# Kernel optimization log

Hardware: AMD Instinct MI355X
Metric: run time of the kernel (lower is better)

The kernel has to match this reference:

```python
import jax, jax.numpy as jnp
import numpy as np

B, S, D = 2, 2048, 1024
H, HD = 16, 64  # num_heads, head_dim; D == H*HD


def setup_inputs() -> dict:
    key = jax.random.key(0)
    k_x, k_wa, k_wp = jax.random.split(key, 3)
    x = jax.random.normal(k_x, (B, S, D), dtype=jnp.float32)
    w_attn = jax.random.normal(k_wa, (D, 3 * D), dtype=jnp.float32) * (1.0 / np.sqrt(D))
    b_attn = jnp.zeros((3 * D,), dtype=jnp.float32)
    w_proj = jax.random.normal(k_wp, (D, D), dtype=jnp.float32) * (1.0 / np.sqrt(D))
    b_proj = jnp.zeros((D,), dtype=jnp.float32)
    return {"x": x, "w_attn": w_attn, "b_attn": b_attn, "w_proj": w_proj, "b_proj": b_proj}


def reference(x, w_attn, b_attn, w_proj, b_proj):
    # c_attn: [B,S,D] -> [B,S,3D], split into q,k,v
    qkv = jnp.einsum('bsd,df->bsf', x, w_attn) + b_attn
    q, k, v = jnp.split(qkv, 3, axis=-1)
    # split heads: [B,S,D] -> [B,S,H,HD]
    q = q.reshape(B, S, H, HD)
    k = k.reshape(B, S, H, HD)
    v = v.reshape(B, S, H, HD)
    scale = 1.0 / jnp.sqrt(jnp.float32(HD))
    # scores: [B,H,S,S]
    scores = jnp.einsum('bnhd,bmhd->bhnm', q, k) * scale
    causal_mask = jnp.tril(jnp.ones((S, S), dtype=jnp.bool_))
    scores = jnp.where(causal_mask, scores, jnp.float32(-1e9))
    attn = jax.nn.softmax(scores, axis=-1)
    # dropout is identity (inference=True / p=0)
    out = jnp.einsum('bhnm,bmhd->bnhd', attn, v)
    out = out.reshape(B, S, D)
    out = jnp.einsum('bsd,de->bse', out, w_proj) + b_proj
    return out
```

## Files before the change

kernel.cpp:

```cpp
#include <hip/hip_runtime.h>

#define Bn 2
#define Sn 2048
#define Dn 1024
#define Hn 16
#define HDn 64

typedef unsigned short u16;
typedef u16 u16x4 __attribute__((ext_vector_type(4)));
typedef u16 u16x8 __attribute__((ext_vector_type(8)));
typedef __bf16 bf16x8 __attribute__((ext_vector_type(8)));
typedef float f32x4 __attribute__((ext_vector_type(4)));

__device__ __forceinline__ u16 f2bf(float f) {
  union { float f; unsigned u; } v; v.f = f;
  unsigned r = v.u + 0x7fffu + ((v.u >> 16) & 1u);
  return (u16)(r >> 16);
}

__device__ __forceinline__ f32x4 mfma16(u16x8 a, u16x8 b, f32x4 c) {
  return __builtin_amdgcn_mfma_f32_16x16x32_bf16(
      __builtin_bit_cast(bf16x8, a), __builtin_bit_cast(bf16x8, b), c, 0, 0, 0);
}

__device__ __forceinline__ int swzb(int row, int bytecol) {
  return row * 128 + (bytecol ^ ((((row & 7) ^ ((row >> 3) & 7))) << 4));
}

__global__ __launch_bounds__(256) void k_cvt(const float* __restrict__ in,
                                             u16* __restrict__ out, int n4) {
  int i = blockIdx.x * 256 + threadIdx.x;
  if (i < n4) {
    const float4 v = reinterpret_cast<const float4*>(in)[i];
    u16x4 o = {f2bf(v.x), f2bf(v.y), f2bf(v.z), f2bf(v.w)};
    reinterpret_cast<u16x4*>(out)[i] = o;
  }
}

__global__ __launch_bounds__(256) void k_transpose(const float* __restrict__ in,
                                                   u16* __restrict__ out,
                                                   int K, int N) {
  __shared__ u16 tile[32][33];
  const int n0 = blockIdx.x * 32, k0 = blockIdx.y * 32;
  const int tx = threadIdx.x, ty = threadIdx.y;
#pragma unroll
  for (int r = 0; r < 4; ++r) {
    const int k = ty * 4 + r;
    tile[k][tx] = f2bf(in[(size_t)(k0 + k) * N + n0 + tx]);
  }
  __syncthreads();
#pragma unroll
  for (int r = 0; r < 4; ++r) {
    const int n = ty * 4 + r;
    out[(size_t)(n0 + n) * K + k0 + tx] = tile[tx][n];
  }
}

__global__ __launch_bounds__(256) void k_gemm_bt(
    const u16* __restrict__ A, const u16* __restrict__ Bt, int K,
    const float* __restrict__ bias, u16* __restrict__ oq, u16* __restrict__ ok,
    u16* __restrict__ ov, float* __restrict__ of, int mode) {
  __shared__ __align__(16) u16 a_lds[128 * 32];
  __shared__ __align__(16) u16 b_lds[128 * 32];
  const int tid = threadIdx.x;
  const int lane = tid & 63, w = tid >> 6;
  const int wr = w >> 1, wc = w & 1;
  const int lm = lane & 15, lk = lane >> 4;
  const int m0 = blockIdx.y * 128, n0 = blockIdx.x * 128;

  f32x4 acc[4][4] = {};

  for (int k0 = 0; k0 < K; k0 += 32) {
#pragma unroll
    for (int p = 0; p < 2; ++p) {
      const int e = p * 2048 + w * 512 + lane * 8;
      const int row = e >> 5, col = e & 31;
      __builtin_amdgcn_global_load_lds(
          (const __attribute__((address_space(1))) void*)(A + (size_t)(m0 + row) * K + k0 + col),
          (__attribute__((address_space(3))) void*)(a_lds + p * 2048 + w * 512),
          16, 0, 0);
      __builtin_amdgcn_global_load_lds(
          (const __attribute__((address_space(1))) void*)(Bt + (size_t)(n0 + row) * K + k0 + col),
          (__attribute__((address_space(3))) void*)(b_lds + p * 2048 + w * 512),
          16, 0, 0);
    }
    __syncthreads();
    u16x8 av[4], bv[4];
#pragma unroll
    for (int m = 0; m < 4; ++m)
      av[m] = *reinterpret_cast<const u16x8*>(a_lds + (wr * 64 + m * 16 + lm) * 32 + lk * 8);
#pragma unroll
    for (int n = 0; n < 4; ++n)
      bv[n] = *reinterpret_cast<const u16x8*>(b_lds + (wc * 64 + n * 16 + lm) * 32 + lk * 8);
#pragma unroll
    for (int m = 0; m < 4; ++m)
#pragma unroll
      for (int n = 0; n < 4; ++n)
        acc[m][n] = mfma16(av[m], bv[n], acc[m][n]);
    __syncthreads();
  }

#pragma unroll
  for (int m = 0; m < 4; ++m) {
#pragma unroll
    for (int n = 0; n < 4; ++n) {
      const int col = n0 + wc * 64 + n * 16 + lm;
      const float bb = bias[col];
#pragma unroll
      for (int j = 0; j < 4; ++j) {
        const int row = m0 + wr * 64 + m * 16 + lk * 4 + j;
        float val = acc[m][n][j] + bb;
        if (mode == 0) {
          const int which = col >> 10;
          const int h = (col >> 6) & 15, hd = col & 63;
          if (which == 0) val *= 0.125f;
          const int b = row >> 11, s = row & 2047;
          const size_t idx = (((size_t)(b * Hn + h)) * Sn + s) * HDn + hd;
          u16* dst = which == 0 ? oq : (which == 1 ? ok : ov);
          dst[idx] = f2bf(val);
        } else {
          of[(size_t)row * Dn + col] = val;
        }
      }
    }
  }
}

__global__ __launch_bounds__(256) void k_attn(const u16* __restrict__ qb,
                                              const u16* __restrict__ kb,
                                              const u16* __restrict__ vb,
                                              u16* __restrict__ ob) {
  const int bx = blockIdx.x;
  const int qt = 31 - (bx >> 5);
  const int bh = bx & 31;
  const int h = bh & 15, b = bh >> 4;
  const int tid = threadIdx.x, lane = tid & 63, w = tid >> 6;
  const int lm = lane & 15, lk = lane >> 4;
  const int Q0 = qt * 64;
  const int q0 = Q0 + w * 16;
  const size_t head = (size_t)(b * Hn + h) * Sn * HDn;
  const u16* Q = qb + head;
  const u16* Kp = kb + head;
  const u16* Vp = vb + head;

  __shared__ __align__(16) u16 k_lds[64 * 64];
  __shared__ __align__(16) u16 vt_lds[64 * 64];
  __shared__ __align__(16) u16 p_lds[4][16 * 64];
  char* myp = (char*)p_lds[w];

  const int sr = tid >> 2, scb = (tid & 3) * 16;
  const u16* Ksrc = Kp + (size_t)sr * HDn + scb;
  const u16* Vsrc = Vp + (size_t)sr * HDn + scb;

  u16x8 aq[2];
#pragma unroll
  for (int c = 0; c < 2; ++c)
    aq[c] = *reinterpret_cast<const u16x8*>(Q + (size_t)(q0 + lm) * HDn + c * 32 + lk * 8);

  f32x4 o_acc[4] = {};
  float mrow = -1e30f, lrow = 0.f;
  const float C = 1.44269504f;

  const int nk = Q0 + 64;
  u16x8 kreg[2], vreg[2];
  kreg[0] = *reinterpret_cast<const u16x8*>(Ksrc);
  kreg[1] = *reinterpret_cast<const u16x8*>(Ksrc + 8);
  vreg[0] = *reinterpret_cast<const u16x8*>(Vsrc);
  vreg[1] = *reinterpret_cast<const u16x8*>(Vsrc + 8);

  for (int j0 = 0; j0 < nk; j0 += 64) {
    *reinterpret_cast<u16x8*>((char*)k_lds + swzb(sr, scb * 2)) = kreg[0];
    *reinterpret_cast<u16x8*>((char*)k_lds + swzb(sr, scb * 2 + 16)) = kreg[1];
#pragma unroll
    for (int i = 0; i < 8; ++i) {
      *reinterpret_cast<u16*>((char*)vt_lds + swzb(scb + i, sr * 2)) = vreg[0][i];
      *reinterpret_cast<u16*>((char*)vt_lds + swzb(scb + 8 + i, sr * 2)) = vreg[1][i];
    }
    __syncthreads();
    if (j0 + 64 < nk) {
      const u16* kn = Ksrc + (size_t)(j0 + 64) * HDn;
      const u16* vn = Vsrc + (size_t)(j0 + 64) * HDn;
      kreg[0] = *reinterpret_cast<const u16x8*>(kn);
      kreg[1] = *reinterpret_cast<const u16x8*>(kn + 8);
      vreg[0] = *reinterpret_cast<const u16x8*>(vn);
      vreg[1] = *reinterpret_cast<const u16x8*>(vn + 8);
    }

    f32x4 s[4];
#pragma unroll
    for (int kc = 0; kc < 4; ++kc) {
      const u16x8 kf0 = *reinterpret_cast<const u16x8*>((char*)k_lds + swzb(kc * 16 + lm, lk * 16));
      const u16x8 kf1 = *reinterpret_cast<const u16x8*>((char*)k_lds + swzb(kc * 16 + lm, 64 + lk * 16));
      f32x4 z = {};
      z = mfma16(kf0, aq[0], z);
      s[kc] = mfma16(kf1, aq[1], z);
    }
    if (j0 + 63 > q0) {
#pragma unroll
      for (int kc = 0; kc < 4; ++kc)
#pragma unroll
        for (int jj = 0; jj < 4; ++jj)
          if (j0 + kc * 16 + lk * 4 + jj > q0 + lm) s[kc][jj] = -1e30f;
    }

    float vmax = -1e30f;
#pragma unroll
    for (int kc = 0; kc < 4; ++kc)
#pragma unroll
      for (int jj = 0; jj < 4; ++jj) vmax = fmaxf(vmax, s[kc][jj]);
    vmax = fmaxf(vmax, __shfl_xor(vmax, 16, 64));
    vmax = fmaxf(vmax, __shfl_xor(vmax, 32, 64));
    const float mnew = fmaxf(mrow, vmax);
    const float alpha = exp2f((mrow - mnew) * C);
    mrow = mnew;
    const float mc = mnew * C;
    float psum = 0.f;
#pragma unroll
    for (int kc = 0; kc < 4; ++kc) {
      u16x4 pk;
#pragma unroll
      for (int jj = 0; jj < 4; ++jj) {
        const float p = exp2f(s[kc][jj] * C - mc);
        psum += p;
        pk[jj] = f2bf(p);
      }
      *reinterpret_cast<u16x4*>(myp + swzb(lm, kc * 32 + lk * 8)) = pk;
    }
    psum += __shfl_xor(psum, 16, 64);
    psum += __shfl_xor(psum, 32, 64);
    lrow = lrow * alpha + psum;

    float a4[4];
#pragma unroll
    for (int jj = 0; jj < 4; ++jj) a4[jj] = __shfl(alpha, lk * 4 + jj, 64);
#pragma unroll
    for (int t = 0; t < 4; ++t)
#pragma unroll
      for (int jj = 0; jj < 4; ++jj) o_acc[t][jj] *= a4[jj];

#pragma unroll
    for (int kt = 0; kt < 2; ++kt) {
      const u16x8 pa = *reinterpret_cast<const u16x8*>(myp + swzb(lm, kt * 64 + lk * 16));
#pragma unroll
      for (int t = 0; t < 4; ++t) {
        const u16x8 vf = *reinterpret_cast<const u16x8*>((char*)vt_lds + swzb(t * 16 + lm, kt * 64 + lk * 16));
        o_acc[t] = mfma16(pa, vf, o_acc[t]);
      }
    }
    __syncthreads();
  }

  float l4[4];
#pragma unroll
  for (int jj = 0; jj < 4; ++jj) l4[jj] = __shfl(lrow, lk * 4 + jj, 64);
#pragma unroll
  for (int t = 0; t < 4; ++t) {
#pragma unroll
    for (int jj = 0; jj < 4; ++jj) {
      const int rowg = q0 + lk * 4 + jj;
      const float val = o_acc[t][jj] / l4[jj];
      ob[((size_t)(b * Sn + rowg)) * Dn + h * HDn + t * 16 + lm] = f2bf(val);
    }
  }
}

extern "C" void kernel_launch(void* const* d_in, const int* in_sizes, int n_in,
                              void* d_out, int out_size, void* d_ws, size_t ws_size,
                              hipStream_t stream) {
  const float* x = (const float*)d_in[0];
  const float* w_attn = (const float*)d_in[1];
  const float* b_attn = (const float*)d_in[2];
  const float* w_proj = (const float*)d_in[3];
  const float* b_proj = (const float*)d_in[4];
  float* out = (float*)d_out;

  u16* ws = (u16*)d_ws;
  u16* xb = ws;
  u16* wat = xb + (size_t)4096 * 1024;
  u16* wpt = wat + (size_t)3072 * 1024;
  u16* qb = wpt + (size_t)1024 * 1024;
  u16* kb = qb + (size_t)Bn * Hn * Sn * HDn;
  u16* vb = kb + (size_t)Bn * Hn * Sn * HDn;
  u16* ao = vb + (size_t)Bn * Hn * Sn * HDn;

  k_cvt<<<4096, 256, 0, stream>>>(x, xb, 1048576);
  k_transpose<<<dim3(3072 / 32, 1024 / 32), dim3(32, 8), 0, stream>>>(w_attn, wat, 1024, 3072);
  k_transpose<<<dim3(1024 / 32, 1024 / 32), dim3(32, 8), 0, stream>>>(w_proj, wpt, 1024, 1024);
  k_gemm_bt<<<dim3(3072 / 128, 4096 / 128), 256, 0, stream>>>(xb, wat, 1024, b_attn, qb, kb, vb, nullptr, 0);
  k_attn<<<Bn * Hn * (Sn / 64), 256, 0, stream>>>(qb, kb, vb, ao);
  k_gemm_bt<<<dim3(1024 / 128, 4096 / 128), 256, 0, stream>>>(ao, wpt, 1024, b_proj, nullptr, nullptr, nullptr, out, 1);
}
```

Baseline: 206.0 us.

## Double-buffer GEMM LDS, lazy softmax rescale, setprio around MFMA, native bf16 cvt

The GEMM kernel gets two LDS buffers so the next K-slice's global-to-LDS loads are issued before the current slice's MFMAs, removing one barrier per iteration. In attention, the running-max rescale of the output accumulators is skipped unless some row's max rises by more than a threshold, and s_setprio raises wave priority around the MFMA sections. The manual float-to-bf16 rounding is replaced by the compiler's native bf16 conversion. Lazy rescaling stays exact but allows larger intermediate exponent values. Double buffering doubles GEMM LDS use, which may lower occupancy.

```diff
diff --git a/kernel.cpp b/kernel.cpp
--- a/kernel.cpp
+++ b/kernel.cpp
@@ -12,10 +12,9 @@
 typedef __bf16 bf16x8 __attribute__((ext_vector_type(8)));
 typedef float f32x4 __attribute__((ext_vector_type(4)));
 
-__device__ __forceinline__ u16 f2bf(float f) {
-  union { float f; unsigned u; } v; v.f = f;
-  unsigned r = v.u + 0x7fffu + ((v.u >> 16) & 1u);
-  return (u16)(r >> 16);
+__device__ __forceinline__ u16 cvt1(float f) {
+  __bf16 h = (__bf16)f;
+  return __builtin_bit_cast(u16, h);
 }
 
 __device__ __forceinline__ f32x4 mfma16(u16x8 a, u16x8 b, f32x4 c) {
@@ -32,7 +31,7 @@
   int i = blockIdx.x * 256 + threadIdx.x;
   if (i < n4) {
     const float4 v = reinterpret_cast<const float4*>(in)[i];
-    u16x4 o = {f2bf(v.x), f2bf(v.y), f2bf(v.z), f2bf(v.w)};
+    u16x4 o = {cvt1(v.x), cvt1(v.y), cvt1(v.z), cvt1(v.w)};
     reinterpret_cast<u16x4*>(out)[i] = o;
   }
 }
@@ -46,7 +45,7 @@
 #pragma unroll
   for (int r = 0; r < 4; ++r) {
     const int k = ty * 4 + r;
-    tile[k][tx] = f2bf(in[(size_t)(k0 + k) * N + n0 + tx]);
+    tile[k][tx] = cvt1(in[(size_t)(k0 + k) * N + n0 + tx]);
   }
   __syncthreads();
 #pragma unroll
@@ -60,8 +59,8 @@
     const u16* __restrict__ A, const u16* __restrict__ Bt, int K,
     const float* __restrict__ bias, u16* __restrict__ oq, u16* __restrict__ ok,
     u16* __restrict__ ov, float* __restrict__ of, int mode) {
-  __shared__ __align__(16) u16 a_lds[128 * 32];
-  __shared__ __align__(16) u16 b_lds[128 * 32];
+  __shared__ __align__(16) u16 a_lds[2][128 * 32];
+  __shared__ __align__(16) u16 b_lds[2][128 * 32];
   const int tid = threadIdx.x;
   const int lane = tid & 63, w = tid >> 6;
   const int wr = w >> 1, wc = w & 1;
@@ -70,35 +69,43 @@
 
   f32x4 acc[4][4] = {};
 
+#define STAGE(d, ko)                                                          \
+  {                                                                           \
+    _Pragma("unroll") for (int p = 0; p < 2; ++p) {                           \
+      const int e = p * 2048 + w * 512 + lane * 8;                            \
+      const int row = e >> 5, col = e & 31;                                   \
+      __builtin_amdgcn_global_load_lds(                                       \
+          (const __attribute__((address_space(1))) void*)(A + (size_t)(m0 + row) * K + (ko) + col), \
+          (__attribute__((address_space(3))) void*)(a_lds[d] + p * 2048 + w * 512), \
+          16, 0, 0);                                                          \
+      __builtin_amdgcn_global_load_lds(                                       \
+          (const __attribute__((address_space(1))) void*)(Bt + (size_t)(n0 + row) * K + (ko) + col), \
+          (__attribute__((address_space(3))) void*)(b_lds[d] + p * 2048 + w * 512), \
+          16, 0, 0);                                                          \
+    }                                                                         \
+  }
+
+  STAGE(0, 0);
+  __syncthreads();
+  int cur = 0;
   for (int k0 = 0; k0 < K; k0 += 32) {
-#pragma unroll
-    for (int p = 0; p < 2; ++p) {
-      const int e = p * 2048 + w * 512 + lane * 8;
-      const int row = e >> 5, col = e & 31;
-      __builtin_amdgcn_global_load_lds(
-          (const __attribute__((address_space(1))) void*)(A + (size_t)(m0 + row) * K + k0 + col),
-          (__attribute__((address_space(3))) void*)(a_lds + p * 2048 + w * 512),
-          16, 0, 0);
-      __builtin_amdgcn_global_load_lds(
-          (const __attribute__((address_space(1))) void*)(Bt + (size_t)(n0 + row) * K + k0 + col),
-          (__attribute__((address_space(3))) void*)(b_lds + p * 2048 + w * 512),
-          16, 0, 0);
-    }
-    __syncthreads();
+    if (k0 + 32 < K) STAGE(cur ^ 1, k0 + 32);
     u16x8 av[4], bv[4];
 #pragma unroll
     for (int m = 0; m < 4; ++m)
-      av[m] = *reinterpret_cast<const u16x8*>(a_lds + (wr * 64 + m * 16 + lm) * 32 + lk * 8);
+      av[m] = *reinterpret_cast<const u16x8*>(a_lds[cur] + (wr * 64 + m * 16 + lm) * 32 + lk * 8);
 #pragma unroll
     for (int n = 0; n < 4; ++n)
-      bv[n] = *reinterpret_cast<const u16x8*>(b_lds + (wc * 64 + n * 16 + lm) * 32 + lk * 8);
+      bv[n] = *reinterpret_cast<const u16x8*>(b_lds[cur] + (wc * 64 + n * 16 + lm) * 32 + lk * 8);
 #pragma unroll
     for (int m = 0; m < 4; ++m)
 #pragma unroll
       for (int n = 0; n < 4; ++n)
         acc[m][n] = mfma16(av[m], bv[n], acc[m][n]);
     __syncthreads();
-  }
+    cur ^= 1;
+  }
+#undef STAGE
 
 #pragma unroll
   for (int m = 0; m < 4; ++m) {
@@ -117,7 +124,7 @@
           const int b = row >> 11, s = row & 2047;
           const size_t idx = (((size_t)(b * Hn + h)) * Sn + s) * HDn + hd;
           u16* dst = which == 0 ? oq : (which == 1 ? ok : ov);
-          dst[idx] = f2bf(val);
+          dst[idx] = cvt1(val);
         } else {
           of[(size_t)row * Dn + col] = val;
         }
@@ -187,6 +194,7 @@
     }
 
     f32x4 s[4];
+    __builtin_amdgcn_s_setprio(1);
 #pragma unroll
     for (int kc = 0; kc < 4; ++kc) {
       const u16x8 kf0 = *reinterpret_cast<const u16x8*>((char*)k_lds + swzb(kc * 16 + lm, lk * 16));
@@ -195,6 +203,7 @@
       z = mfma16(kf0, aq[0], z);
       s[kc] = mfma16(kf1, aq[1], z);
     }
+    __builtin_amdgcn_s_setprio(0);
     if (j0 + 63 > q0) {
 #pragma unroll
       for (int kc = 0; kc < 4; ++kc)
@@ -210,10 +219,20 @@
       for (int jj = 0; jj < 4; ++jj) vmax = fmaxf(vmax, s[kc][jj]);
     vmax = fmaxf(vmax, __shfl_xor(vmax, 16, 64));
     vmax = fmaxf(vmax, __shfl_xor(vmax, 32, 64));
-    const float mnew = fmaxf(mrow, vmax);
-    const float alpha = exp2f((mrow - mnew) * C);
-    mrow = mnew;
-    const float mc = mnew * C;
+    if (!__all(vmax - mrow <= 8.0f)) {
+      const float mnew = fmaxf(mrow, vmax);
+      const float alpha = exp2f((mrow - mnew) * C);
+      mrow = mnew;
+      lrow *= alpha;
+      float a4[4];
+#pragma unroll
+      for (int jj = 0; jj < 4; ++jj) a4[jj] = __shfl(alpha, lk * 4 + jj, 64);
+#pragma unroll
+      for (int t = 0; t < 4; ++t)
+#pragma unroll
+        for (int jj = 0; jj < 4; ++jj) o_acc[t][jj] *= a4[jj];
+    }
+    const float mc = mrow * C;
     float psum = 0.f;
 #pragma unroll
     for (int kc = 0; kc < 4; ++kc) {
@@ -222,22 +241,15 @@
       for (int jj = 0; jj < 4; ++jj) {
         const float p = exp2f(s[kc][jj] * C - mc);
         psum += p;
-        pk[jj] = f2bf(p);
+        pk[jj] = cvt1(p);
       }
       *reinterpret_cast<u16x4*>(myp + swzb(lm, kc * 32 + lk * 8)) = pk;
     }
     psum += __shfl_xor(psum, 16, 64);
     psum += __shfl_xor(psum, 32, 64);
-    lrow = lrow * alpha + psum;
-
-    float a4[4];
-#pragma unroll
-    for (int jj = 0; jj < 4; ++jj) a4[jj] = __shfl(alpha, lk * 4 + jj, 64);
-#pragma unroll
-    for (int t = 0; t < 4; ++t)
-#pragma unroll
-      for (int jj = 0; jj < 4; ++jj) o_acc[t][jj] *= a4[jj];
-
+    lrow += psum;
+
+    __builtin_amdgcn_s_setprio(1);
 #pragma unroll
     for (int kt = 0; kt < 2; ++kt) {
       const u16x8 pa = *reinterpret_cast<const u16x8*>(myp + swzb(lm, kt * 64 + lk * 16));
@@ -247,6 +259,7 @@
         o_acc[t] = mfma16(pa, vf, o_acc[t]);
       }
     }
+    __builtin_amdgcn_s_setprio(0);
     __syncthreads();
   }
 
@@ -259,7 +272,7 @@
     for (int jj = 0; jj < 4; ++jj) {
       const int rowg = q0 + lk * 4 + jj;
       const float val = o_acc[t][jj] / l4[jj];
-      ob[((size_t)(b * Sn + rowg)) * Dn + h * HDn + t * 16 + lm] = f2bf(val);
+      ob[((size_t)(b * Sn + rowg)) * Dn + h * HDn + t * 16 + lm] = cvt1(val);
     }
   }
 }
```

After: 202.8 us. About the same (-1.5%).
